# Kernel tuning notes

Measured on AMD Instinct MI355X. Metric: run time of the kernel, lower is better.

Reference implementation:

```python
import jax, jax.numpy as jnp
import numpy as np

N = 50000   # nodes
E = 640000  # edges
IN = 128    # input feature dim (== H*C so every layer has a residual)
H = 4       # heads
C = 32      # out channels per head
L = 3       # layers
D = H * C   # 128, per-layer output width
NEG_SLOPE = 0.2
LN_EPS = 1e-5


def setup_inputs() -> dict:
    key = jax.random.key(0)
    ks = jax.random.split(key, 6)
    s = 0.1  # keep activations well-scaled
    x = jax.random.normal(ks[0], (N, IN), dtype=jnp.float32)
    edge_index = jax.random.randint(ks[1], (2, E), 0, N)
    Wl = jax.random.normal(ks[2], (L, IN, D), dtype=jnp.float32) * s
    bl = jnp.zeros((L, D), dtype=jnp.float32)
    Wr = jax.random.normal(ks[3], (L, IN, D), dtype=jnp.float32) * s
    br = jnp.zeros((L, D), dtype=jnp.float32)
    att = jax.random.normal(ks[4], (L, H, C), dtype=jnp.float32) * s
    bias = jnp.zeros((L, D), dtype=jnp.float32)
    gamma = jnp.ones((L, D), dtype=jnp.float32)
    beta = jnp.zeros((L, D), dtype=jnp.float32)
    return {"x": x, "edge_index": edge_index, "Wl": Wl, "bl": bl,
            "Wr": Wr, "br": br, "att": att, "bias": bias,
            "gamma": gamma, "beta": beta}


def _gatv2_layer(x, src, dst, Wl, bl, Wr, br, att, bias):
    # GATv2Conv (concat heads, eval mode so attention dropout is identity)
    xl = (x @ Wl + bl).reshape(N, H, C)  # source transform
    xr = (x @ Wr + br).reshape(N, H, C)  # target transform
    # edge-wise gather: message along edge j->i uses xl[j] + xr[i]
    e = jax.nn.leaky_relu(xl[src] + xr[dst], NEG_SLOPE)      # [E,H,C]
    logit = jnp.einsum('ehc,hc->eh', e, att)                  # [E,H]
    # segment softmax over incoming edges of each target node
    m = jax.ops.segment_max(logit, dst, num_segments=N)       # [N,H]
    a = jnp.exp(logit - m[dst])
    denom = jax.ops.segment_sum(a, dst, num_segments=N)       # [N,H]
    a = a / (denom[dst] + 1e-16)
    # scatter-aggregate weighted source messages
    out = jax.ops.segment_sum(a[:, :, None] * xl[src], dst, num_segments=N)
    return out.reshape(N, D) + bias


def _layer_norm(h, g, b):
    mu = jnp.mean(h, axis=-1, keepdims=True)
    var = jnp.mean((h - mu) ** 2, axis=-1, keepdims=True)
    return (h - mu) * jax.lax.rsqrt(var + LN_EPS) * g + b


def reference(x, edge_index, Wl, bl, Wr, br, att, bias, gamma, beta):
    src, dst = edge_index[0], edge_index[1]
    out = x
    for l in range(L):  # small fixed layer count
        h = jax.nn.relu(_gatv2_layer(out, src, dst, Wl[l], bl[l], Wr[l], br[l], att[l], bias[l]))
        h = _layer_norm(h, gamma[l], beta[l])
        out = h + out  # in_dim == hidden*heads, so residual at every layer
    return out
```

## Files before the change

kernel.cpp:

```cpp
#include <hip/hip_runtime.h>
#include <hip/hip_bf16.h>
#include <math.h>

#define N_NODES 50000
#define N_EDGES 640000
#define DIM 128
#define NLAYER 3
#define LN_EPS 1e-5f
#define LOG2E 1.44269504088896f
#define NSCAN 49

#if __has_builtin(__builtin_amdgcn_exp2f)
#define EXP2(x) __builtin_amdgcn_exp2f(x)
#else
#define EXP2(x) exp2f(x)
#endif

typedef __attribute__((ext_vector_type(8))) short bf16x8;
typedef __attribute__((ext_vector_type(4))) float f32x4;

__device__ inline ushort f2b(float f) {
    __hip_bfloat16 h = __float2bfloat16(f);
    return *reinterpret_cast<ushort*>(&h);
}
__device__ inline float bf_lo(unsigned u) { return __uint_as_float(u << 16); }
__device__ inline float bf_hi(unsigned u) { return __uint_as_float(u & 0xffff0000u); }
__device__ inline float lr(float t) { return fmaf(0.4f, fabsf(t), 0.6f * t); }
__device__ inline unsigned pack2(float a, float b) {
    return (unsigned)f2b(a) | ((unsigned)f2b(b) << 16);
}
__device__ inline int cw_of(int w) { return (w & 15) + 32 * (w >> 4); }

template<int CTRL>
__device__ inline float dppadd(float v) {
    int m = __builtin_amdgcn_update_dpp(0, __float_as_int(v), CTRL, 0xF, 0xF, true);
    return v + __int_as_float(m);
}
__device__ inline float reduce16(float v) {
    v = dppadd<0x124>(v);
    v = dppadd<0x128>(v);
    v = dppadd<0xB1>(v);
    v = dppadd<0x4E>(v);
    return v;
}


__global__ __launch_bounds__(256) void zerofill(int4* __restrict__ p, int n4) {
    int i = blockIdx.x * 256 + threadIdx.x;
    if (i < n4) p[i] = make_int4(0, 0, 0, 0);
}


__global__ __launch_bounds__(256) void fusedinit(
    const float* __restrict__ x, unsigned* __restrict__ curb,
    const float* __restrict__ Wl, const float* __restrict__ Wr, ushort* __restrict__ Wt,
    const int* __restrict__ dst, int* __restrict__ deg,
    const float* __restrict__ att, const float* __restrict__ bias,
    const float* __restrict__ gamma, const float* __restrict__ beta,
    float2* __restrict__ params)
{
    int b = blockIdx.x, t = threadIdx.x;
    if (b < 12500) {
        int i = b * 256 + t;
        int node = i >> 6, w = i & 63;
        int c = cw_of(w);
        curb[i] = pack2(x[node * DIM + c], x[node * DIM + c + 16]);
    } else if (b < 12884) {
        int i = (b - 12500) * 256 + t;
        if (i < NLAYER * 2 * DIM * DIM) {
            int p = i & 127, n = (i >> 7) & 127, mat = (i >> 14) & 1, l = i >> 15;
            int c = cw_of(p >> 1) + (p & 1) * 16;
            const float* W = mat ? Wr : Wl;
            Wt[i] = f2b(W[l * DIM * DIM + c * DIM + n]);
        }
    } else if (b < 15384) {
        int e = (b - 12884) * 256 + t;
        atomicAdd(&deg[dst[e]], 1);
    } else {
        int i = t;
        if (i < NLAYER * 64) {
            int l = i >> 6, w = i & 63;
            int c = cw_of(w);
            const float* A = att + l * DIM;
            const float* B = bias + l * DIM;
            const float* G = gamma + l * DIM;
            const float* E = beta + l * DIM;
            params[l * 256 + w]       = make_float2(A[c] * LOG2E, A[c + 16] * LOG2E);
            params[l * 256 + 64 + w]  = make_float2(B[c], B[c + 16]);
            params[l * 256 + 128 + w] = make_float2(G[c], G[c + 16]);
            params[l * 256 + 192 + w] = make_float2(E[c], E[c + 16]);
        }
    }
}


__global__ __launch_bounds__(1024) void scan1(const int* __restrict__ deg,
                                              int* __restrict__ rowptr,
                                              int* __restrict__ bsum,
                                              int* __restrict__ blockhist) {
    __shared__ int sd[1024];
    __shared__ int lh[256];
    int t = threadIdx.x;
    int idx = blockIdx.x * 1024 + t;
    if (t < 256) lh[t] = 0;
    __syncthreads();
    int v = (idx < N_NODES) ? deg[idx] : 0;
    if (idx < N_NODES) atomicAdd(&lh[v < 255 ? v : 255], 1);
    sd[t] = v;
    __syncthreads();
    for (int off = 1; off < 1024; off <<= 1) {
        int add = (t >= off) ? sd[t - off] : 0;
        __syncthreads();
        sd[t] += add;
        __syncthreads();
    }
    if (idx < N_NODES) rowptr[idx + 1] = sd[t];
    if (t == 1023) bsum[blockIdx.x] = sd[1023];
    if (t < 256) blockhist[blockIdx.x * 256 + t] = lh[t];
}

__global__ __launch_bounds__(1024) void midscan(const int* __restrict__ bsum,
                                                int* __restrict__ bcarry,
                                                const int* __restrict__ blockhist,
                                                int* __restrict__ bboff) {
    __shared__ int sh[256];
    int t = threadIdx.x;
    if (t < 256) {
        int tot = 0;
        for (int b = 0; b < NSCAN; ++b) tot += blockhist[b * 256 + t];
        sh[t] = tot;
    }
    __syncthreads();
    for (int off = 1; off < 256; off <<= 1) {
        int add = 0;
        if (t < 256 && t >= off) add = sh[t - off];
        __syncthreads();
        if (t < 256) sh[t] += add;
        __syncthreads();
    }
    if (t < 256) {
        int run = sh[255] - sh[t];
        for (int b = 0; b < NSCAN; ++b) {
            bboff[b * 256 + t] = run;
            run += blockhist[b * 256 + t];
        }
    }
    if (t == 0) {
        int c = 0;
        for (int b = 0; b < NSCAN; ++b) { bcarry[b] = c; c += bsum[b]; }
    }
}

__global__ __launch_bounds__(1024) void scan2(int* __restrict__ rowptr,
                                              const int* __restrict__ bcarry,
                                              const int* __restrict__ deg,
                                              const int* __restrict__ bboff,
                                              int* __restrict__ order) {
    __shared__ int lh[256];
    int t = threadIdx.x;
    int idx = blockIdx.x * 1024 + t;
    if (t < 256) lh[t] = 0;
    __syncthreads();
    int carry = bcarry[blockIdx.x];
    if (idx == 0) rowptr[0] = 0;
    if (idx < N_NODES) {
        rowptr[idx + 1] += carry;
        int d = deg[idx];
        int bin = d < 255 ? d : 255;
        int rank = atomicAdd(&lh[bin], 1);
        order[bboff[blockIdx.x * 256 + bin] + rank] = idx;
    }
}

__global__ void scatter_kernel(const int* __restrict__ src, const int* __restrict__ dst,
                               const int* __restrict__ rowptr, int* __restrict__ cnt,
                               int* __restrict__ esrc,
                               const int* __restrict__ order, const int* __restrict__ deg,
                               int4* __restrict__ slotinfo) {
    int e = blockIdx.x * blockDim.x + threadIdx.x;
    if (e < N_EDGES) {
        int d = dst[e];
        int pos = rowptr[d] + atomicAdd(&cnt[d], 1);
        esrc[pos] = src[e] << 8;
    }
    if (e < N_NODES) {
        int nd = order[e];
        int r0 = rowptr[nd];
        slotinfo[e] = make_int4(nd, r0, r0 + deg[nd], 0);
    }
}


__global__ __launch_bounds__(256) void gemm_mfma(
    const ushort* __restrict__ A,
    const ushort* __restrict__ Wt_l,
    const float* __restrict__ bl, const float* __restrict__ br,
    unsigned* __restrict__ xlb, unsigned* __restrict__ xrb)
{
    int mat = blockIdx.y;
    int rowbase = blockIdx.x * 128;
    int wid = threadIdx.x >> 6;
    int lane = threadIdx.x & 63;
    int wr = wid >> 1, wc = wid & 1;
    int m0 = rowbase + wr * 64, n0 = wc * 64;

    const ushort* W = Wt_l + mat * DIM * DIM;
    const float* bias = mat ? br : bl;
    unsigned* out = mat ? xrb : xlb;

    int fr = lane & 15;
    int kg = lane >> 4;

    bf16x8 af[4][4], bfr[4][4];
    #pragma unroll
    for (int mf = 0; mf < 4; ++mf) {
        int row = m0 + mf * 16 + fr;
        if (row > N_NODES - 1) row = N_NODES - 1;
        const ushort* p = A + (size_t)row * DIM + kg * 8;
        #pragma unroll
        for (int kf = 0; kf < 4; ++kf)
            af[mf][kf] = *reinterpret_cast<const bf16x8*>(p + kf * 32);
    }
    #pragma unroll
    for (int nf = 0; nf < 4; ++nf) {
        const ushort* p = W + (size_t)(n0 + nf * 16 + fr) * DIM + kg * 8;
        #pragma unroll
        for (int kf = 0; kf < 4; ++kf)
            bfr[nf][kf] = *reinterpret_cast<const bf16x8*>(p + kf * 32);
    }

    f32x4 acc[4][4];
    #pragma unroll
    for (int mf = 0; mf < 4; ++mf)
        #pragma unroll
        for (int nf = 0; nf < 4; ++nf)
            acc[mf][nf] = (f32x4){0.f, 0.f, 0.f, 0.f};

    #pragma unroll
    for (int kf = 0; kf < 4; ++kf)
        #pragma unroll
        for (int mf = 0; mf < 4; ++mf)
            #pragma unroll
            for (int nf = 0; nf < 4; ++nf)
                acc[mf][nf] = __builtin_amdgcn_mfma_f32_16x16x32_bf16(
                    af[mf][kf], bfr[nf][kf], acc[mf][nf], 0, 0, 0);

    int col = lane & 15;
    int r4 = lane >> 4;
    float bb[4];
    #pragma unroll
    for (int nf = 0; nf < 4; ++nf) bb[nf] = bias[n0 + nf * 16 + col];

    #pragma unroll
    for (int mf = 0; mf < 4; ++mf) {
        #pragma unroll
        for (int pj = 0; pj < 2; ++pj) {
            int w = col + 32 * wc + 16 * pj;
            #pragma unroll
            for (int r = 0; r < 4; ++r) {
                int row = m0 + mf * 16 + r4 * 4 + r;
                if (row < N_NODES)
                    out[(size_t)row * 64 + w] =
                        pack2(acc[mf][2 * pj][r] + bb[2 * pj],
                              acc[mf][2 * pj + 1][r] + bb[2 * pj + 1]);
            }
        }
    }
}


__device__ inline void gather8(const char* __restrict__ xb, int laneoff,
                               const int j[8], unsigned u[8]) {
    #pragma unroll
    for (int i = 0; i < 8; ++i)
        u[i] = *(const unsigned*)(xb + j[i] + laneoff);
}

__device__ inline void compute8(const unsigned u[8], float ax, float ay,
                                float xrx, float xry,
                                float& s, float& ox, float& oy) {
    #pragma unroll
    for (int i = 0; i < 8; ++i) {
        float vx = bf_lo(u[i]), vy = bf_hi(u[i]);
        float p = lr(vx + xrx) * ax + lr(vy + xry) * ay;
        p = reduce16(p);
        float w = EXP2(p);
        s += w; ox = fmaf(w, vx, ox); oy = fmaf(w, vy, oy);
    }
}

__device__ inline void computeT(const unsigned u[8], float ax, float ay,
                                float xrx, float xry,
                                float& s, float& ox, float& oy, int rem) {
    #pragma unroll
    for (int i = 0; i < 8; ++i) {
        if (i < rem) {
            float vx = bf_lo(u[i]), vy = bf_hi(u[i]);
            float p = lr(vx + xrx) * ax + lr(vy + xry) * ay;
            p = reduce16(p);
            float w = EXP2(p);
            s += w; ox = fmaf(w, vx, ox); oy = fmaf(w, vy, oy);
        }
    }
}

__global__ __launch_bounds__(256) void agg_kernel(
    const unsigned* __restrict__ xlb2, const unsigned* __restrict__ xrb2,
    const int* __restrict__ esrc, const int4* __restrict__ slotinfo,
    const float2* __restrict__ P4,
    unsigned* __restrict__ curb, float* __restrict__ outf, int last)
{
    int slot = blockIdx.x * 4 + (threadIdx.x >> 6);
    int lane = threadIdx.x & 63;
    int4 si = slotinfo[slot];
    int node = __builtin_amdgcn_readfirstlane(si.x);
    int e0   = __builtin_amdgcn_readfirstlane(si.y);
    int e1   = __builtin_amdgcn_readfirstlane(si.z);

    unsigned xru = xrb2[node * 64 + lane];
    float2 att2 = P4[lane];
    float2 b2   = P4[64 + lane];
    float2 g2   = P4[128 + lane];
    float2 be2  = P4[192 + lane];
    unsigned old = curb[node * 64 + lane];
    float xrx = bf_lo(xru), xry = bf_hi(xru);

    const char* xb = (const char*)xlb2;
    int laneoff = lane << 2;

    float s = 0.f, ox = 0.f, oy = 0.f;
    int nb = (e1 - e0) >> 3;
    int rem = (e1 - e0) & 7;

    int jc[8], jn[8];
    unsigned uc[8], un[8];

    if (nb > 0) {
        #pragma unroll
        for (int i = 0; i < 8; ++i) jc[i] = esrc[e0 + i];
        gather8(xb, laneoff, jc, uc);
    }
    int ec = e0;
    for (int b = 1; b < nb; ++b) {
        int en = ec + 8;
        #pragma unroll
        for (int i = 0; i < 8; ++i) jn[i] = esrc[en + i];
        gather8(xb, laneoff, jn, un);
        compute8(uc, att2.x, att2.y, xrx, xry, s, ox, oy);
        #pragma unroll
        for (int i = 0; i < 8; ++i) uc[i] = un[i];
        ec = en;
    }
    if (nb > 0) {
        if (rem) {
            int et = ec + 8;
            #pragma unroll
            for (int i = 0; i < 8; ++i)
                jn[i] = esrc[et + (i < rem ? i : rem - 1)];
            gather8(xb, laneoff, jn, un);
            compute8(uc, att2.x, att2.y, xrx, xry, s, ox, oy);
            computeT(un, att2.x, att2.y, xrx, xry, s, ox, oy, rem);
        } else {
            compute8(uc, att2.x, att2.y, xrx, xry, s, ox, oy);
        }
    } else if (rem) {
        #pragma unroll
        for (int i = 0; i < 8; ++i)
            jc[i] = esrc[e0 + (i < rem ? i : rem - 1)];
        gather8(xb, laneoff, jc, uc);
        computeT(uc, att2.x, att2.y, xrx, xry, s, ox, oy, rem);
    }

    float inv = 1.f / (s + 1e-16f);
    float gx = fmaxf(fmaf(ox, inv, b2.x), 0.f);
    float gy = fmaxf(fmaf(oy, inv, b2.y), 0.f);

    float sum = gx + gy;
    sum = reduce16(sum);
    sum += __shfl_xor(sum, 16);
    sum += __shfl_xor(sum, 32);
    float mu = sum * (1.f / 128.f);
    float dx = gx - mu, dy = gy - mu;
    float ss = dx * dx + dy * dy;
    ss = reduce16(ss);
    ss += __shfl_xor(ss, 16);
    ss += __shfl_xor(ss, 32);
    float rstd = rsqrtf(ss * (1.f / 128.f) + LN_EPS);

    float yx = fmaf(dx * rstd, g2.x, be2.x) + bf_lo(old);
    float yy = fmaf(dy * rstd, g2.y, be2.y) + bf_hi(old);

    if (last) {
        int c = cw_of(lane);
        outf[node * DIM + c] = yx;
        outf[node * DIM + c + 16] = yy;
    } else {
        curb[node * 64 + lane] = pack2(yx, yy);
    }
}


extern "C" void kernel_launch(void* const* d_in, const int* in_sizes, int n_in,
                              void* d_out, int out_size, void* d_ws, size_t ws_size,
                              hipStream_t stream) {
    const float* x     = (const float*)d_in[0];
    const int*   ei    = (const int*)d_in[1];
    const float* Wl    = (const float*)d_in[2];
    const float* bl    = (const float*)d_in[3];
    const float* Wr    = (const float*)d_in[4];
    const float* br    = (const float*)d_in[5];
    const float* att   = (const float*)d_in[6];
    const float* bias  = (const float*)d_in[7];
    const float* gamma = (const float*)d_in[8];
    const float* beta  = (const float*)d_in[9];
    float* outf = (float*)d_out;

    char* ws = (char*)d_ws;
    size_t off = 0;
    auto alloc = [&](size_t bytes) -> void* {
        void* p = ws + off;
        off += (bytes + 255) & ~size_t(255);
        return p;
    };
    unsigned* curb = (unsigned*)alloc((size_t)N_NODES * 64 * 4);
    unsigned* xlb  = (unsigned*)alloc((size_t)N_NODES * 64 * 4);
    unsigned* xrb  = (unsigned*)alloc((size_t)N_NODES * 64 * 4);
    ushort* Wt     = (ushort*)alloc((size_t)NLAYER * 2 * DIM * DIM * 2);
    int* esrc      = (int*)alloc((size_t)N_EDGES * 4);
    int* rowptr    = (int*)alloc((size_t)(N_NODES + 1) * 4);
    int* zbase     = (int*)alloc((size_t)(2 * N_NODES + 2 * 64) * 4);
    int* deg = zbase, *cnt = zbase + N_NODES;
    int* bsum = cnt + N_NODES, *bcarry = bsum + 64;
    int* blockhist = (int*)alloc((size_t)NSCAN * 256 * 4);
    int* bboff     = (int*)alloc((size_t)NSCAN * 256 * 4);
    int* order     = (int*)alloc((size_t)N_NODES * 4);
    int4* slotinfo = (int4*)alloc((size_t)N_NODES * 16);
    float2* params = (float2*)alloc((size_t)NLAYER * 256 * sizeof(float2));

    const int* srcArr = ei;
    const int* dstArr = ei + N_EDGES;

    int n4 = (2 * N_NODES + 2 * 64) / 4;
    zerofill<<<(n4 + 255) / 256, 256, 0, stream>>>((int4*)zbase, n4);
    fusedinit<<<15385, 256, 0, stream>>>(x, curb, Wl, Wr, Wt, dstArr, deg,
                                         att, bias, gamma, beta, params);
    scan1<<<NSCAN, 1024, 0, stream>>>(deg, rowptr, bsum, blockhist);
    midscan<<<1, 1024, 0, stream>>>(bsum, bcarry, blockhist, bboff);
    scan2<<<NSCAN, 1024, 0, stream>>>(rowptr, bcarry, deg, bboff, order);
    scatter_kernel<<<(N_EDGES + 255) / 256, 256, 0, stream>>>(
        srcArr, dstArr, rowptr, cnt, esrc, order, deg, slotinfo);

    for (int l = 0; l < NLAYER; ++l) {
        gemm_mfma<<<dim3((N_NODES + 127) / 128, 2), 256, 0, stream>>>(
            (const ushort*)curb, Wt + (size_t)l * 2 * DIM * DIM,
            bl + (size_t)l * DIM, br + (size_t)l * DIM, xlb, xrb);
        agg_kernel<<<12500, 256, 0, stream>>>(
            xlb, xrb, esrc, slotinfo, params + (size_t)l * 256,
            curb, outf, l == NLAYER - 1 ? 1 : 0);
    }
}
```

Baseline: 270.0 us.

## Fuse edge scatter into first-layer GEMM launch and double-buffer GEMM K loads

The CSR scatter kernel is merged into the first layer's GEMM launch as extra blocks, so the scatter and GEMM work share one grid and can run concurrently instead of back to back. The GEMM's 2D grid becomes a flattened 1D grid. Its operand loads also change from preloading all K fragments to a two-stage register double buffer, which cuts register pressure and overlaps loads with MFMA. The risks are block-scheduling imbalance in the mixed grid and the scatter blocks delaying the GEMM blocks.

```diff
diff --git a/kernel.cpp b/kernel.cpp
--- a/kernel.cpp
+++ b/kernel.cpp
@@ -9,6 +9,8 @@
 #define LN_EPS 1e-5f
 #define LOG2E 1.44269504088896f
 #define NSCAN 49
+#define NG 391
+#define SCATB 2500
 
 #if __has_builtin(__builtin_amdgcn_exp2f)
 #define EXP2(x) __builtin_amdgcn_exp2f(x)
@@ -172,35 +174,40 @@
     }
 }
 
-__global__ void scatter_kernel(const int* __restrict__ src, const int* __restrict__ dst,
-                               const int* __restrict__ rowptr, int* __restrict__ cnt,
-                               int* __restrict__ esrc,
-                               const int* __restrict__ order, const int* __restrict__ deg,
-                               int4* __restrict__ slotinfo) {
-    int e = blockIdx.x * blockDim.x + threadIdx.x;
-    if (e < N_EDGES) {
-        int d = dst[e];
-        int pos = rowptr[d] + atomicAdd(&cnt[d], 1);
-        esrc[pos] = src[e] << 8;
-    }
-    if (e < N_NODES) {
-        int nd = order[e];
-        int r0 = rowptr[nd];
-        slotinfo[e] = make_int4(nd, r0, r0 + deg[nd], 0);
-    }
-}
-
-
-__global__ __launch_bounds__(256) void gemm_mfma(
+
+__global__ __launch_bounds__(256) void gemm_sc(
     const ushort* __restrict__ A,
     const ushort* __restrict__ Wt_l,
     const float* __restrict__ bl, const float* __restrict__ br,
-    unsigned* __restrict__ xlb, unsigned* __restrict__ xrb)
+    unsigned* __restrict__ xlb, unsigned* __restrict__ xrb,
+    int do_scat,
+    const int* __restrict__ src, const int* __restrict__ dst,
+    const int* __restrict__ rowptr, int* __restrict__ cnt,
+    int* __restrict__ esrc,
+    const int* __restrict__ order, const int* __restrict__ deg,
+    int4* __restrict__ slotinfo)
 {
-    int mat = blockIdx.y;
-    int rowbase = blockIdx.x * 128;
-    int wid = threadIdx.x >> 6;
-    int lane = threadIdx.x & 63;
+    int b = blockIdx.x, t = threadIdx.x;
+    if (do_scat) {
+        if (b < SCATB) {
+            int e = b * 256 + t;
+            int d = dst[e];
+            int pos = rowptr[d] + atomicAdd(&cnt[d], 1);
+            esrc[pos] = src[e] << 8;
+            if (e < N_NODES) {
+                int nd = order[e];
+                int r0 = rowptr[nd];
+                slotinfo[e] = make_int4(nd, r0, r0 + deg[nd], 0);
+            }
+            return;
+        }
+        b -= SCATB;
+    }
+
+    int mat = b >= NG;
+    int rowbase = (mat ? b - NG : b) * 128;
+    int wid = t >> 6;
+    int lane = t & 63;
     int wr = wid >> 1, wc = wid & 1;
     int m0 = rowbase + wr * 64, n0 = wc * 64;
 
@@ -211,23 +218,23 @@
     int fr = lane & 15;
     int kg = lane >> 4;
 
-    bf16x8 af[4][4], bfr[4][4];
+    const ushort* pa[4];
     #pragma unroll
     for (int mf = 0; mf < 4; ++mf) {
         int row = m0 + mf * 16 + fr;
         if (row > N_NODES - 1) row = N_NODES - 1;
-        const ushort* p = A + (size_t)row * DIM + kg * 8;
-        #pragma unroll
-        for (int kf = 0; kf < 4; ++kf)
-            af[mf][kf] = *reinterpret_cast<const bf16x8*>(p + kf * 32);
-    }
-    #pragma unroll
-    for (int nf = 0; nf < 4; ++nf) {
-        const ushort* p = W + (size_t)(n0 + nf * 16 + fr) * DIM + kg * 8;
-        #pragma unroll
-        for (int kf = 0; kf < 4; ++kf)
-            bfr[nf][kf] = *reinterpret_cast<const bf16x8*>(p + kf * 32);
-    }
+        pa[mf] = A + (size_t)row * DIM + kg * 8;
+    }
+    const ushort* pb[4];
+    #pragma unroll
+    for (int nf = 0; nf < 4; ++nf)
+        pb[nf] = W + (size_t)(n0 + nf * 16 + fr) * DIM + kg * 8;
+
+    bf16x8 af[2][4], bfr[2][4];
+    #pragma unroll
+    for (int mf = 0; mf < 4; ++mf) af[0][mf] = *reinterpret_cast<const bf16x8*>(pa[mf]);
+    #pragma unroll
+    for (int nf = 0; nf < 4; ++nf) bfr[0][nf] = *reinterpret_cast<const bf16x8*>(pb[nf]);
 
     f32x4 acc[4][4];
     #pragma unroll
@@ -237,13 +244,23 @@
             acc[mf][nf] = (f32x4){0.f, 0.f, 0.f, 0.f};
 
     #pragma unroll
-    for (int kf = 0; kf < 4; ++kf)
+    for (int kf = 0; kf < 4; ++kf) {
+        int cur = kf & 1, nxt = cur ^ 1;
+        if (kf < 3) {
+            #pragma unroll
+            for (int mf = 0; mf < 4; ++mf)
+                af[nxt][mf] = *reinterpret_cast<const bf16x8*>(pa[mf] + (kf + 1) * 32);
+            #pragma unroll
+            for (int nf = 0; nf < 4; ++nf)
+                bfr[nxt][nf] = *reinterpret_cast<const bf16x8*>(pb[nf] + (kf + 1) * 32);
+        }
         #pragma unroll
         for (int mf = 0; mf < 4; ++mf)
             #pragma unroll
             for (int nf = 0; nf < 4; ++nf)
                 acc[mf][nf] = __builtin_amdgcn_mfma_f32_16x16x32_bf16(
-                    af[mf][kf], bfr[nf][kf], acc[mf][nf], 0, 0, 0);
+                    af[cur][mf], bfr[cur][nf], acc[mf][nf], 0, 0, 0);
+    }
 
     int col = lane & 15;
     int r4 = lane >> 4;
@@ -447,13 +464,14 @@
     scan1<<<NSCAN, 1024, 0, stream>>>(deg, rowptr, bsum, blockhist);
     midscan<<<1, 1024, 0, stream>>>(bsum, bcarry, blockhist, bboff);
     scan2<<<NSCAN, 1024, 0, stream>>>(rowptr, bcarry, deg, bboff, order);
-    scatter_kernel<<<(N_EDGES + 255) / 256, 256, 0, stream>>>(
-        srcArr, dstArr, rowptr, cnt, esrc, order, deg, slotinfo);
 
     for (int l = 0; l < NLAYER; ++l) {
-        gemm_mfma<<<dim3((N_NODES + 127) / 128, 2), 256, 0, stream>>>(
+        int do_scat = (l == 0) ? 1 : 0;
+        int grid = 2 * NG + (do_scat ? SCATB : 0);
+        gemm_sc<<<grid, 256, 0, stream>>>(
             (const ushort*)curb, Wt + (size_t)l * 2 * DIM * DIM,
-            bl + (size_t)l * DIM, br + (size_t)l * DIM, xlb, xrb);
+            bl + (size_t)l * DIM, br + (size_t)l * DIM, xlb, xrb,
+            do_scat, srcArr, dstArr, rowptr, cnt, esrc, order, deg, slotinfo);
         agg_kernel<<<12500, 256, 0, stream>>>(
             xlb, xrb, esrc, slotinfo, params + (size_t)l * 256,
             curb, outf, l == NLAYER - 1 ? 1 : 0);
```

Measured after the change: 264.4 us. 2.1% less time.
